# Kernel tuning notes

Hardware: AMD Instinct MI355X
Metric: run time of the kernel (lower is better)

The kernel has to match this reference:

```python
import jax, jax.numpy as jnp
import numpy as np

B, L, D = 8, 512, 256


def hard_sigmoid(x):
    # Keras 1.x default inner_activation for LSTM gates
    return jnp.clip(0.2 * x + 0.5, 0.0, 1.0)


def lstm_step(x_t, h, c, W, U, b):
    # gates in Keras order: i, f, g(candidate), o
    z = x_t @ W + h @ U + b  # (B, 4D)
    i, f, g, o = jnp.split(z, 4, axis=-1)
    i = hard_sigmoid(i)
    f = hard_sigmoid(f)
    g = jnp.tanh(g)
    o = hard_sigmoid(o)
    c_new = f * c + i * g
    h_new = o * jnp.tanh(c_new)
    return h_new, c_new


def setup_inputs() -> dict:
    key = jax.random.key(0)
    ks = jax.random.split(key, 10)
    s = 1.0 / np.sqrt(D)
    x = jax.random.normal(ks[0], (B, L, D), dtype=jnp.float32)
    W_r = jax.random.normal(ks[1], (D, 4 * D), dtype=jnp.float32) * s
    U_r = jax.random.normal(ks[2], (D, 4 * D), dtype=jnp.float32) * s
    b_r = jnp.zeros((4 * D,), dtype=jnp.float32)
    W_w = jax.random.normal(ks[3], (D, 4 * D), dtype=jnp.float32) * s
    U_w = jax.random.normal(ks[4], (D, 4 * D), dtype=jnp.float32) * s
    b_w = jnp.zeros((4 * D,), dtype=jnp.float32)
    W_c = jax.random.normal(ks[5], (2 * D, D), dtype=jnp.float32) * s
    b_c = jnp.zeros((D,), dtype=jnp.float32)
    return {"x": x, "W_r": W_r, "U_r": U_r, "b_r": b_r,
            "W_w": W_w, "U_w": U_w, "b_w": b_w, "W_c": W_c, "b_c": b_c}


def reference(x, W_r, U_r, b_r, W_w, U_w, b_w, W_c, b_c):
    Bb, Ll, Dd = x.shape
    h0 = jnp.zeros((Bb, Dd), dtype=x.dtype)

    # --- reader LSTM (return_sequences=True), eq. 1 ---
    def reader_step(carry, x_t):
        h, c = carry
        h, c = lstm_step(x_t, h, c, W_r, U_r, b_r)
        return (h, c), h

    _, o_seq = jax.lax.scan(reader_step, (h0, h0), jnp.swapaxes(x, 0, 1))  # (L, B, D)

    # --- compose-and-write loop, eqs. 2-6; mem_0 = x ---
    def write_step(carry, o_t):
        mem, h, c = carry  # mem: (B, L, D)
        z = jax.nn.softmax(jnp.einsum('bd,bld->bl', o_t, mem), axis=-1)  # (B, L)
        m_rt = jnp.einsum('bl,bld->bd', z, mem)                           # (B, D)
        c_t = jnp.concatenate([o_t, m_rt], axis=-1) @ W_c + b_c          # linear composer
        h_new, c_new = lstm_step(c_t, h, c, W_w, U_w, b_w)
        mem_new = mem * (1.0 - z[..., None]) + h_new[:, None, :] * z[..., None]
        return (mem_new, h_new, c_new), h_new

    (_, _, _), h_seq = jax.lax.scan(write_step, (x, h0, h0), o_seq)
    # return_mode == 'last_output'
    return h_seq[-1]
```

## Files before the change

kernel.cpp:

```cpp
#include <hip/hip_runtime.h>
#include <math.h>

#define BB 8
#define LL 512
#define DD 256
#define NG4 1024
#define WGB 32
#define WR 16
#define WU 8
#define MLD 264

typedef __attribute__((ext_vector_type(4))) float f32x4;

static const size_t OFF_XW    = 0;
static const size_t OFF_F     = OFF_XW + (size_t)BB*LL*NG4;
static const size_t OFF_BMW   = OFF_F + (size_t)DD*NG4;
static const size_t OFF_B2    = OFF_BMW + (size_t)DD*NG4;
static const size_t OFF_HR    = OFF_B2 + NG4;
static const size_t OFF_HW    = OFF_HR + (size_t)2*BB*DD;
static const size_t OFF_PMAX  = OFF_HW + (size_t)BB*DD;
static const size_t OFF_PSUM  = OFF_PMAX + (size_t)BB*WGB;
static const size_t OFF_PM    = OFF_PSUM + (size_t)BB*WGB;
static const size_t OFF_FLAGS = OFF_PM + (size_t)BB*WGB*DD;
static const size_t TOTAL_WS  = OFF_FLAGS + BB*WGB;

__device__ __forceinline__ float hsig(float x) {
    return fminf(fmaxf(0.2f*x + 0.5f, 0.0f), 1.0f);
}

__device__ __forceinline__ void st_coh(float* p, float v) {
    __hip_atomic_store(p, v, __ATOMIC_RELAXED, __HIP_MEMORY_SCOPE_AGENT);
}
__device__ __forceinline__ float ld_coh(const float* p) {
    return __hip_atomic_load(p, __ATOMIC_RELAXED, __HIP_MEMORY_SCOPE_AGENT);
}
__device__ __forceinline__ void st_coh_u(unsigned* p, unsigned v) {
    __hip_atomic_store(p, v, __ATOMIC_RELAXED, __HIP_MEMORY_SCOPE_AGENT);
}
__device__ __forceinline__ unsigned ld_coh_u(const unsigned* p) {
    return __hip_atomic_load(p, __ATOMIC_RELAXED, __HIP_MEMORY_SCOPE_AGENT);
}

__device__ __forceinline__ void ld_pm8(
    const f32x4* p0, const f32x4* p1, const f32x4* p2, const f32x4* p3,
    const f32x4* p4, const f32x4* p5, const f32x4* p6, const f32x4* p7,
    f32x4& a0, f32x4& a1, f32x4& a2, f32x4& a3,
    f32x4& a4, f32x4& a5, f32x4& a6, f32x4& a7)
{
    asm volatile(
        "global_load_dwordx4 %0, %8, off sc0 sc1\n\t"
        "global_load_dwordx4 %1, %9, off sc0 sc1\n\t"
        "global_load_dwordx4 %2, %10, off sc0 sc1\n\t"
        "global_load_dwordx4 %3, %11, off sc0 sc1\n\t"
        "global_load_dwordx4 %4, %12, off sc0 sc1\n\t"
        "global_load_dwordx4 %5, %13, off sc0 sc1\n\t"
        "global_load_dwordx4 %6, %14, off sc0 sc1\n\t"
        "global_load_dwordx4 %7, %15, off sc0 sc1\n\t"
        "s_waitcnt vmcnt(0)"
        : "=&v"(a0), "=&v"(a1), "=&v"(a2), "=&v"(a3),
          "=&v"(a4), "=&v"(a5), "=&v"(a6), "=&v"(a7)
        : "v"(p0), "v"(p1), "v"(p2), "v"(p3),
          "v"(p4), "v"(p5), "v"(p6), "v"(p7)
        : "memory");
}

__device__ __forceinline__ void flag_barrier(unsigned* flb, int wg, unsigned target, int tid) {
    asm volatile("s_waitcnt vmcnt(0)" ::: "memory");
    __syncthreads();
    if (tid == 0) st_coh_u(&flb[wg], target);
    if (tid < 64) {
        unsigned v;
        do {
            v = ld_coh_u(&flb[tid & 31]);
        } while (!__all(v >= target));
    }
    __syncthreads();
}

template<int TM, int TN, int TK>
__global__ void __launch_bounds__(256) gemm_nn(
    const float* __restrict__ A, int lda,
    const float* __restrict__ Bmat, int ldb,
    const float* __restrict__ bias,
    float* __restrict__ C, int ldc,
    int M, int N, int K)
{
    __shared__ float As[TK][TM];
    __shared__ float Bs[TK][TN];
    const int m0 = blockIdx.y * TM, n0 = blockIdx.x * TN;
    const int tid = threadIdx.x;
    const int tx = tid % (TN/4);
    const int ty = tid / (TN/4);
    float acc[4][4] = {};
    for (int k0 = 0; k0 < K; k0 += TK) {
        {
            const int e = tid*4;
            const int m = e / TK, k = e % TK;
            const float4 v = *reinterpret_cast<const float4*>(&A[(size_t)(m0+m)*lda + k0 + k]);
            As[k+0][m] = v.x; As[k+1][m] = v.y; As[k+2][m] = v.z; As[k+3][m] = v.w;
        }
        {
            const int e = tid*4;
            const int k = e / TN, n = e % TN;
            const float4 v = *reinterpret_cast<const float4*>(&Bmat[(size_t)(k0+k)*ldb + n0 + n]);
            Bs[k][n+0] = v.x; Bs[k][n+1] = v.y; Bs[k][n+2] = v.z; Bs[k][n+3] = v.w;
        }
        __syncthreads();
        #pragma unroll
        for (int kk = 0; kk < TK; ++kk) {
            float a[4], bv[4];
            #pragma unroll
            for (int i = 0; i < 4; ++i) a[i] = As[kk][ty*4+i];
            #pragma unroll
            for (int j = 0; j < 4; ++j) bv[j] = Bs[kk][tx*4+j];
            #pragma unroll
            for (int i = 0; i < 4; ++i)
                #pragma unroll
                for (int j = 0; j < 4; ++j) acc[i][j] += a[i]*bv[j];
        }
        __syncthreads();
    }
    #pragma unroll
    for (int i = 0; i < 4; ++i) {
        const int m = m0 + ty*4 + i;
        #pragma unroll
        for (int j = 0; j < 4; ++j) {
            const int n = n0 + tx*4 + j;
            C[(size_t)m*ldc + n] = acc[i][j] + (bias ? bias[n] : 0.0f);
        }
    }
}

__global__ void __launch_bounds__(256) b2_kernel(
    const float* __restrict__ bc, const float* __restrict__ Ww,
    const float* __restrict__ bw, float* __restrict__ B2)
{
    const int n = blockIdx.x*256 + threadIdx.x;
    float a = bw[n];
    for (int k = 0; k < DD; ++k) a += bc[k]*Ww[(size_t)k*NG4 + n];
    B2[n] = a;
}

__global__ void __launch_bounds__(256) fused_kernel(
    const float* __restrict__ XW, const float* __restrict__ Fw,
    const float* __restrict__ Bm, const float* __restrict__ B2,
    const float* __restrict__ Ur, const float* __restrict__ Uw,
    const float* __restrict__ x,
    float* __restrict__ HR, float* __restrict__ HWb,
    float* __restrict__ PMAX, float* __restrict__ PSUM, float* __restrict__ PM,
    unsigned* __restrict__ flags, float* __restrict__ out)
{
    extern __shared__ float sm[];
    float* Urs  = sm;
    float* Uws  = Urs + 8192;
    float* Fs   = Uws + 8192;
    float* Bms  = Fs + 8192;
    float* mems = Bms + 8192;
    float* hr   = mems + WR*MLD;
    float* hw   = hr + 256;
    float* ms   = hw + 256;
    float* zredR= ms + 256;
    float* zredW= zredR + 256;
    float* red4 = zredW + 256;
    float* xws  = red4 + 1024;
    float* zrs  = xws + 32;
    float* g1s  = zrs + 32;
    float* zws  = g1s + 32;
    float* b2s  = zws + 32;
    float* fwS  = b2s + 32;
    float* ssx  = fwS + 32;
    float* esx  = ssx + 16;
    float* cr   = esx + 16;
    float* cw   = cr + 8;
    float* misc = cw + 8;

    const int b   = (int)blockIdx.x & 7;
    const int wg  = (int)blockIdx.x >> 3;
    const int tid = threadIdx.x;
    const int R0  = wg*WR;
    const int U0  = wg*WU;

    for (int it = 0; it < 32; ++it) {
        const int e = it*256 + tid;
        const int k = e >> 5, cl = e & 31;
        const int gc = (cl>>3)*DD + U0 + (cl&7);
        Urs[k*32+cl] = Ur[(size_t)k*NG4 + gc];
        Uws[k*32+cl] = Uw[(size_t)k*NG4 + gc];
        Fs [k*32+cl] = Fw[(size_t)k*NG4 + gc];
        Bms[k*32+cl] = Bm[(size_t)k*NG4 + gc];
    }
    if (tid < 32) b2s[tid] = B2[(tid>>3)*DD + U0 + (tid&7)];
    for (int r = 0; r < WR; ++r)
        mems[r*MLD + tid] = x[((size_t)b*LL + R0 + r)*DD + tid];
    if (tid < 8) { cr[tid] = 0.f; cw[tid] = 0.f; }
    __syncthreads();

    unsigned* flb = flags + b*WGB;

    for (int s = 0; s <= LL; ++s) {
        const bool doR = (s < LL), doW = (s >= 1);

        if (doR && tid < 32)
            xws[tid] = XW[((size_t)b*LL + s)*NG4 + (tid>>3)*DD + U0 + (tid&7)];
        hr[tid] = (s >= 1) ? ld_coh(&HR[((size_t)((s-1)&1))*BB*DD + b*DD + tid]) : 0.f;
        hw[tid] = (s >= 2) ? ld_coh(&HWb[b*DD + tid]) : 0.f;
        __syncthreads();

        if (s >= 2) {
            const float scale = misc[0];
            const float hwd = hw[tid];
            #pragma unroll
            for (int r = 0; r < WR; ++r) {
                const float z = esx[r]*scale;
                float* mp = &mems[r*MLD + tid];
                *mp = *mp*(1.f - z) + hwd*z;
            }
        }
        __syncthreads();

        if (doW) {
            const int r = tid >> 4, j = tid & 15;
            float a = 0.f;
            const float* mrow = mems + r*MLD;
            #pragma unroll 4
            for (int d = j; d < DD; d += 16) a += hr[d]*mrow[d];
            #pragma unroll
            for (int off = 8; off; off >>= 1) a += __shfl_down(a, off, 16);
            if (j == 0) ssx[r] = a;
        }
        {
            const int kc = tid >> 5, cl = tid & 31;
            const int k0 = kc*32;
            float aR = 0.f, aW = 0.f;
            #pragma unroll 8
            for (int k = k0; k < k0+32; ++k) {
                aR += hr[k]*Urs[k*32+cl];
                aW += hw[k]*Uws[k*32+cl] + hr[k]*Fs[k*32+cl];
            }
            zredR[tid] = aR; zredW[tid] = aW;
        }
        __syncthreads();

        if (tid < 16) {
            const float v = ssx[tid];
            float m = v;
            #pragma unroll
            for (int off = 8; off; off >>= 1) m = fmaxf(m, __shfl_xor(m, off, 16));
            const float e = __expf(v - m);
            esx[tid] = e;
            float sum = e;
            #pragma unroll
            for (int off = 8; off; off >>= 1) sum += __shfl_xor(sum, off, 16);
            if (tid == 0 && doW) {
                st_coh(&PMAX[b*WGB + wg], m);
                st_coh(&PSUM[b*WGB + wg], sum);
            }
        } else if (tid >= 64 && tid < 96) {
            const int cl = tid - 64;
            float z = xws[cl];
            #pragma unroll
            for (int q = 0; q < 8; ++q) z += zredR[q*32 + cl];
            zrs[cl] = z;
        } else if (tid >= 128 && tid < 160) {
            const int cl = tid - 128;
            float z = b2s[cl];
            #pragma unroll
            for (int q = 0; q < 8; ++q) z += zredW[q*32 + cl];
            g1s[cl] = z;
        }
        __syncthreads();

        if (doW) {
            float p = 0.f;
            #pragma unroll
            for (int r = 0; r < WR; ++r) p += esx[r]*mems[r*MLD + tid];
            st_coh(&PM[((size_t)b*WGB + wg)*DD + tid], p);
        }
        if (doR && tid < 8) {
            const float ig = hsig(zrs[tid]);
            const float fg = hsig(zrs[8+tid]);
            const float gg = tanhf(zrs[16+tid]);
            const float og = hsig(zrs[24+tid]);
            const float c  = fg*cr[tid] + ig*gg;
            cr[tid] = c;
            st_coh(&HR[((size_t)(s&1))*BB*DD + b*DD + U0 + tid], og*tanhf(c));
        }
        flag_barrier(flb, wg, 2u*(unsigned)s + 1u, tid);

        if (doW) {
            if (tid < 32) {
                const float pmx = ld_coh(&PMAX[b*WGB + tid]);
                const float ps  = ld_coh(&PSUM[b*WGB + tid]);
                float g = pmx;
                #pragma unroll
                for (int off = 16; off; off >>= 1) g = fmaxf(g, __shfl_xor(g, off, 32));
                const float fw = __expf(pmx - g);
                float S = ps*fw;
                #pragma unroll
                for (int off = 16; off; off >>= 1) S += __shfl_xor(S, off, 32);
                fwS[tid] = fw;
                if (tid == 0)  misc[1] = 1.f/S;
                if (tid == wg) misc[0] = fw/S;
            }
            __syncthreads();
            {
                const int w0 = tid >> 6, dq = tid & 63;
                const float* pmb = PM + (size_t)b*WGB*DD;
                const f32x4* p0 = (const f32x4*)(pmb + (w0+ 0)*DD) + dq;
                const f32x4* p1 = (const f32x4*)(pmb + (w0+ 4)*DD) + dq;
                const f32x4* p2 = (const f32x4*)(pmb + (w0+ 8)*DD) + dq;
                const f32x4* p3 = (const f32x4*)(pmb + (w0+12)*DD) + dq;
                const f32x4* p4 = (const f32x4*)(pmb + (w0+16)*DD) + dq;
                const f32x4* p5 = (const f32x4*)(pmb + (w0+20)*DD) + dq;
                const f32x4* p6 = (const f32x4*)(pmb + (w0+24)*DD) + dq;
                const f32x4* p7 = (const f32x4*)(pmb + (w0+28)*DD) + dq;
                f32x4 a0,a1,a2,a3,a4,a5,a6,a7;
                ld_pm8(p0,p1,p2,p3,p4,p5,p6,p7, a0,a1,a2,a3,a4,a5,a6,a7);
                f32x4 acc = a0*fwS[w0];
                acc += a1*fwS[w0+4];  acc += a2*fwS[w0+8];
                acc += a3*fwS[w0+12]; acc += a4*fwS[w0+16];
                acc += a5*fwS[w0+20]; acc += a6*fwS[w0+24];
                acc += a7*fwS[w0+28];
                *(f32x4*)(red4 + w0*DD + dq*4) = acc;
            }
            __syncthreads();
            ms[tid] = (red4[tid] + red4[DD+tid] + red4[2*DD+tid] + red4[3*DD+tid]) * misc[1];
            __syncthreads();
            {
                const int kc = tid >> 5, cl = tid & 31, k0 = kc*32;
                float a = 0.f;
                #pragma unroll 8
                for (int k = k0; k < k0+32; ++k) a += ms[k]*Bms[k*32+cl];
                zredW[tid] = a;
            }
            __syncthreads();
            if (tid < 32) {
                float z = g1s[tid];
                #pragma unroll
                for (int q = 0; q < 8; ++q) z += zredW[q*32 + tid];
                zws[tid] = z;
            }
            __syncthreads();
            if (tid < 8) {
                const float ig = hsig(zws[tid]);
                const float fg = hsig(zws[8+tid]);
                const float gg = tanhf(zws[16+tid]);
                const float og = hsig(zws[24+tid]);
                const float c  = fg*cw[tid] + ig*gg;
                cw[tid] = c;
                const float h = og*tanhf(c);
                st_coh(&HWb[b*DD + U0 + tid], h);
                if (s == LL) out[b*DD + U0 + tid] = h;
            }
        }
        if (s < LL) flag_barrier(flb, wg, 2u*(unsigned)s + 2u, tid);
    }
}

extern "C" void kernel_launch(void* const* d_in, const int* in_sizes, int n_in,
                              void* d_out, int out_size, void* d_ws, size_t ws_size,
                              hipStream_t stream) {
    const float* x   = (const float*)d_in[0];
    const float* W_r = (const float*)d_in[1];
    const float* U_r = (const float*)d_in[2];
    const float* b_r = (const float*)d_in[3];
    const float* W_w = (const float*)d_in[4];
    const float* U_w = (const float*)d_in[5];
    const float* b_w = (const float*)d_in[6];
    const float* W_c = (const float*)d_in[7];
    const float* b_c = (const float*)d_in[8];
    (void)in_sizes; (void)n_in;

    if (ws_size < TOTAL_WS * sizeof(float)) return;

    float* ws   = (float*)d_ws;
    float* XW   = ws + OFF_XW;
    float* Fmat = ws + OFF_F;
    float* Bmw  = ws + OFF_BMW;
    float* B2   = ws + OFF_B2;
    float* HR   = ws + OFF_HR;
    float* HWb  = ws + OFF_HW;
    float* PMAX = ws + OFF_PMAX;
    float* PSUM = ws + OFF_PSUM;
    float* PM   = ws + OFF_PM;
    unsigned* flags = (unsigned*)(ws + OFF_FLAGS);

    const int FUSED_LDS = 39540 * 4;
    hipFuncSetAttribute((const void*)fused_kernel, hipFuncAttributeMaxDynamicSharedMemorySize, FUSED_LDS);

    hipMemsetAsync(flags, 0, BB*WGB*sizeof(unsigned), stream);

    dim3 blk(256);
    gemm_nn<64,64,16><<<dim3(NG4/64, (BB*LL)/64), blk, 0, stream>>>(
        x, DD, W_r, NG4, b_r, XW, NG4, BB*LL, NG4, DD);
    gemm_nn<64,64,16><<<dim3(NG4/64, DD/64), blk, 0, stream>>>(
        W_c, DD, W_w, NG4, nullptr, Fmat, NG4, DD, NG4, DD);
    gemm_nn<64,64,16><<<dim3(NG4/64, DD/64), blk, 0, stream>>>(
        W_c + (size_t)DD*DD, DD, W_w, NG4, nullptr, Bmw, NG4, DD, NG4, DD);
    b2_kernel<<<dim3(NG4/256), blk, 0, stream>>>(b_c, W_w, b_w, B2);
    fused_kernel<<<dim3(BB*WGB), blk, FUSED_LDS, stream>>>(
        XW, Fmat, Bmw, B2, U_r, U_w, x, HR, HWb, PMAX, PSUM, PM, flags, (float*)d_out);
}
```

Baseline: 4.711 ms.

## Restructure fused LSTM step to overlap reader with writer and shorten barrier paths

Reorganizes the per-step schedule of the persistent fused kernel. The reader LSTM runs one step ahead, and its first step is computed directly at setup. The attention score is computed algebraically from the previous dot product plus a single h·hw reduction, which avoids reading the updated memory first. The memory update is moved into the flag-barrier wait window, and the global loads for PM, PMAX/PSUM, HR and XW are issued right after the barrier so they overlap. The aim is to take LDS passes and barrier latency off the serial critical path, at the cost of more complex indexing and a higher risk of subtle ordering or correctness bugs.

```diff
diff --git a/kernel.cpp b/kernel.cpp
--- a/kernel.cpp
+++ b/kernel.cpp
@@ -64,19 +64,6 @@
         : "memory");
 }
 
-__device__ __forceinline__ void flag_barrier(unsigned* flb, int wg, unsigned target, int tid) {
-    asm volatile("s_waitcnt vmcnt(0)" ::: "memory");
-    __syncthreads();
-    if (tid == 0) st_coh_u(&flb[wg], target);
-    if (tid < 64) {
-        unsigned v;
-        do {
-            v = ld_coh_u(&flb[tid & 31]);
-        } while (!__all(v >= target));
-    }
-    __syncthreads();
-}
-
 template<int TM, int TN, int TK>
 __global__ void __launch_bounds__(256) gemm_nn(
     const float* __restrict__ A, int lda,
@@ -156,21 +143,23 @@
     float* Fs   = Uws + 8192;
     float* Bms  = Fs + 8192;
     float* mems = Bms + 8192;
-    float* hr   = mems + WR*MLD;
-    float* hw   = hr + 256;
+    float* hr2  = mems + WR*MLD;
+    float* hw   = hr2 + 512;
     float* ms   = hw + 256;
     float* zredR= ms + 256;
     float* zredW= zredR + 256;
     float* red4 = zredW + 256;
     float* xws  = red4 + 1024;
-    float* zrs  = xws + 32;
-    float* g1s  = zrs + 32;
-    float* zws  = g1s + 32;
-    float* b2s  = zws + 32;
-    float* fwS  = b2s + 32;
-    float* ssx  = fwS + 32;
-    float* esx  = ssx + 16;
-    float* cr   = esx + 16;
+    float* b2s  = xws + 32;
+    float* zrs  = b2s + 32;
+    float* zws  = zrs + 32;
+    float* fwS  = zws + 32;
+    float* d1   = fwS + 32;
+    float* zp   = d1 + 16;
+    float* esx  = zp + 16;
+    float* wv   = esx + 16;
+    float* wsum = wv + 16;
+    float* cr   = wsum + 8;
     float* cw   = cr + 8;
     float* misc = cw + 8;
 
@@ -179,6 +168,7 @@
     const int tid = threadIdx.x;
     const int R0  = wg*WR;
     const int U0  = wg*WU;
+    const int gc32 = (tid>>3)*DD + U0 + (tid&7);
 
     for (int it = 0; it < 32; ++it) {
         const int e = it*256 + tid;
@@ -189,113 +179,123 @@
         Fs [k*32+cl] = Fw[(size_t)k*NG4 + gc];
         Bms[k*32+cl] = Bm[(size_t)k*NG4 + gc];
     }
-    if (tid < 32) b2s[tid] = B2[(tid>>3)*DD + U0 + (tid&7)];
+    if (tid < 32) b2s[tid] = B2[gc32];
     for (int r = 0; r < WR; ++r)
         mems[r*MLD + tid] = x[((size_t)b*LL + R0 + r)*DD + tid];
-    if (tid < 8) { cr[tid] = 0.f; cw[tid] = 0.f; }
+    {
+        const size_t base = (size_t)b*LL*NG4;
+        const float zi = XW[base + tid];
+        const float zg = XW[base + 512 + tid];
+        const float zo = XW[base + 768 + tid];
+        const float c0 = hsig(zi)*tanhf(zg);
+        hr2[tid] = hsig(zo)*tanhf(c0);
+        hr2[256 + tid] = 0.f;
+        if (tid >= U0 && tid < U0+WU) cr[tid-U0] = c0;
+    }
+    if (tid < 16) { zp[tid] = 0.f; d1[tid] = 0.f; esx[tid] = 0.f; }
+    if (tid < 8)  cw[tid] = 0.f;
+    if (tid < 4)  misc[tid] = 0.f;
     __syncthreads();
 
     unsigned* flb = flags + b*WGB;
 
     for (int s = 0; s <= LL; ++s) {
-        const bool doR = (s < LL), doW = (s >= 1);
-
-        if (doR && tid < 32)
-            xws[tid] = XW[((size_t)b*LL + s)*NG4 + (tid>>3)*DD + U0 + (tid&7)];
-        hr[tid] = (s >= 1) ? ld_coh(&HR[((size_t)((s-1)&1))*BB*DD + b*DD + tid]) : 0.f;
-        hw[tid] = (s >= 2) ? ld_coh(&HWb[b*DD + tid]) : 0.f;
-        __syncthreads();
-
-        if (s >= 2) {
-            const float scale = misc[0];
-            const float hwd = hw[tid];
-            #pragma unroll
-            for (int r = 0; r < WR; ++r) {
-                const float z = esx[r]*scale;
-                float* mp = &mems[r*MLD + tid];
-                *mp = *mp*(1.f - z) + hwd*z;
-            }
-        }
-        __syncthreads();
-
-        if (doW) {
-            const int r = tid >> 4, j = tid & 15;
-            float a = 0.f;
-            const float* mrow = mems + r*MLD;
-            #pragma unroll 4
-            for (int d = j; d < DD; d += 16) a += hr[d]*mrow[d];
-            #pragma unroll
-            for (int off = 8; off; off >>= 1) a += __shfl_down(a, off, 16);
-            if (j == 0) ssx[r] = a;
-        }
+        const bool doW = (s >= 1);
+        float* hrN_s = hr2 + (s&1)*256;
+        float* hrO_s = hr2 + ((s+1)&1)*256;
+
+        float hw_r = 0.f;
+        if (s >= 2) hw_r = ld_coh(&HWb[b*DD + tid]);
+        hw[tid] = hw_r;
+        __syncthreads();
+
         {
-            const int kc = tid >> 5, cl = tid & 31;
-            const int k0 = kc*32;
-            float aR = 0.f, aW = 0.f;
-            #pragma unroll 8
-            for (int k = k0; k < k0+32; ++k) {
-                aR += hr[k]*Urs[k*32+cl];
-                aW += hw[k]*Uws[k*32+cl] + hr[k]*Fs[k*32+cl];
-            }
-            zredR[tid] = aR; zredW[tid] = aW;
-        }
-        __syncthreads();
-
-        if (tid < 16) {
-            const float v = ssx[tid];
-            float m = v;
+            float v = hrO_s[tid]*hw_r;
+            #pragma unroll
+            for (int off = 32; off; off >>= 1) v += __shfl_xor(v, off);
+            if ((tid & 63) == 0) wsum[tid>>6] = v;
+        }
+        __syncthreads();
+
+        if (doW && tid < 16) {
+            const float d2v = wsum[0]+wsum[1]+wsum[2]+wsum[3];
+            const float zpv = zp[tid];
+            const float sc  = (1.f - zpv)*d1[tid] + zpv*d2v;
+            float m = sc;
             #pragma unroll
             for (int off = 8; off; off >>= 1) m = fmaxf(m, __shfl_xor(m, off, 16));
-            const float e = __expf(v - m);
+            const float e = __expf(sc - m);
             esx[tid] = e;
-            float sum = e;
-            #pragma unroll
-            for (int off = 8; off; off >>= 1) sum += __shfl_xor(sum, off, 16);
-            if (tid == 0 && doW) {
+            wv[tid]  = e*(1.f - zpv);
+            float sum = e, bp = e*zpv;
+            #pragma unroll
+            for (int off = 8; off; off >>= 1) {
+                sum += __shfl_xor(sum, off, 16);
+                bp  += __shfl_xor(bp,  off, 16);
+            }
+            if (tid == 0) {
+                misc[2] = bp;
                 st_coh(&PMAX[b*WGB + wg], m);
                 st_coh(&PSUM[b*WGB + wg], sum);
             }
-        } else if (tid >= 64 && tid < 96) {
-            const int cl = tid - 64;
-            float z = xws[cl];
-            #pragma unroll
-            for (int q = 0; q < 8; ++q) z += zredR[q*32 + cl];
-            zrs[cl] = z;
-        } else if (tid >= 128 && tid < 160) {
-            const int cl = tid - 128;
-            float z = b2s[cl];
-            #pragma unroll
-            for (int q = 0; q < 8; ++q) z += zredW[q*32 + cl];
-            g1s[cl] = z;
         }
         __syncthreads();
 
         if (doW) {
-            float p = 0.f;
-            #pragma unroll
-            for (int r = 0; r < WR; ++r) p += esx[r]*mems[r*MLD + tid];
+            float p = misc[2]*hw_r;
+            #pragma unroll
+            for (int r = 0; r < WR; ++r) p += wv[r]*mems[r*MLD + tid];
             st_coh(&PM[((size_t)b*WGB + wg)*DD + tid], p);
         }
-        if (doR && tid < 8) {
-            const float ig = hsig(zrs[tid]);
-            const float fg = hsig(zrs[8+tid]);
-            const float gg = tanhf(zrs[16+tid]);
-            const float og = hsig(zrs[24+tid]);
-            const float c  = fg*cr[tid] + ig*gg;
-            cr[tid] = c;
-            st_coh(&HR[((size_t)(s&1))*BB*DD + b*DD + U0 + tid], og*tanhf(c));
-        }
-        flag_barrier(flb, wg, 2u*(unsigned)s + 1u, tid);
+
+        asm volatile("s_waitcnt vmcnt(0)" ::: "memory");
+        __syncthreads();
+        if (tid == 0) st_coh_u(&flb[wg], 2u*(unsigned)s + 1u);
+        if (s >= 2) {
+            #pragma unroll
+            for (int r = 0; r < WR; ++r) {
+                const float z = zp[r];
+                float* mp = &mems[r*MLD + tid];
+                *mp = *mp*(1.f - z) + hw_r*z;
+            }
+        }
+        if (tid < 64) {
+            const unsigned target = 2u*(unsigned)s + 1u;
+            unsigned v;
+            do { v = ld_coh_u(&flb[tid & 31]); } while (!__all(v >= target));
+        }
+        __syncthreads();
+
+        float hrN_r = 0.f;
+        if (s >= 1 && s <= 511) hrN_r = ld_coh(&HR[((size_t)(s&1))*BB*DD + b*DD + tid]);
+        float xw_r = 0.f;
+        if (s <= 510 && tid < 32) xw_r = XW[((size_t)b*LL + s + 1)*NG4 + gc32];
+        float pmx_r = 0.f, ps_r = 0.f;
+        if (doW && tid < 32) {
+            pmx_r = ld_coh(&PMAX[b*WGB + tid]);
+            ps_r  = ld_coh(&PSUM[b*WGB + tid]);
+        }
+        f32x4 a0,a1,a2,a3,a4,a5,a6,a7;
+        const int w0 = tid >> 6, dq = tid & 63;
+        if (doW) {
+            const float* pmb = PM + (size_t)b*WGB*DD;
+            ld_pm8((const f32x4*)(pmb + (w0+ 0)*DD) + dq, (const f32x4*)(pmb + (w0+ 4)*DD) + dq,
+                   (const f32x4*)(pmb + (w0+ 8)*DD) + dq, (const f32x4*)(pmb + (w0+12)*DD) + dq,
+                   (const f32x4*)(pmb + (w0+16)*DD) + dq, (const f32x4*)(pmb + (w0+20)*DD) + dq,
+                   (const f32x4*)(pmb + (w0+24)*DD) + dq, (const f32x4*)(pmb + (w0+28)*DD) + dq,
+                   a0,a1,a2,a3,a4,a5,a6,a7);
+        }
+        if (s >= 1 && s <= 511) hrN_s[tid] = hrN_r;
+        if (s <= 510 && tid < 32) xws[tid] = xw_r;
+        __syncthreads();
 
         if (doW) {
             if (tid < 32) {
-                const float pmx = ld_coh(&PMAX[b*WGB + tid]);
-                const float ps  = ld_coh(&PSUM[b*WGB + tid]);
-                float g = pmx;
+                float g = pmx_r;
                 #pragma unroll
                 for (int off = 16; off; off >>= 1) g = fmaxf(g, __shfl_xor(g, off, 32));
-                const float fw = __expf(pmx - g);
-                float S = ps*fw;
+                const float fw = __expf(pmx_r - g);
+                float S = ps_r*fw;
                 #pragma unroll
                 for (int off = 16; off; off >>= 1) S += __shfl_xor(S, off, 32);
                 fwS[tid] = fw;
@@ -304,18 +304,6 @@
             }
             __syncthreads();
             {
-                const int w0 = tid >> 6, dq = tid & 63;
-                const float* pmb = PM + (size_t)b*WGB*DD;
-                const f32x4* p0 = (const f32x4*)(pmb + (w0+ 0)*DD) + dq;
-                const f32x4* p1 = (const f32x4*)(pmb + (w0+ 4)*DD) + dq;
-                const f32x4* p2 = (const f32x4*)(pmb + (w0+ 8)*DD) + dq;
-                const f32x4* p3 = (const f32x4*)(pmb + (w0+12)*DD) + dq;
-                const f32x4* p4 = (const f32x4*)(pmb + (w0+16)*DD) + dq;
-                const f32x4* p5 = (const f32x4*)(pmb + (w0+20)*DD) + dq;
-                const f32x4* p6 = (const f32x4*)(pmb + (w0+24)*DD) + dq;
-                const f32x4* p7 = (const f32x4*)(pmb + (w0+28)*DD) + dq;
-                f32x4 a0,a1,a2,a3,a4,a5,a6,a7;
-                ld_pm8(p0,p1,p2,p3,p4,p5,p6,p7, a0,a1,a2,a3,a4,a5,a6,a7);
                 f32x4 acc = a0*fwS[w0];
                 acc += a1*fwS[w0+4];  acc += a2*fwS[w0+8];
                 acc += a3*fwS[w0+12]; acc += a4*fwS[w0+16];
@@ -325,17 +313,19 @@
             }
             __syncthreads();
             ms[tid] = (red4[tid] + red4[DD+tid] + red4[2*DD+tid] + red4[3*DD+tid]) * misc[1];
+            if (tid < 16) zp[tid] = esx[tid]*misc[0];
             __syncthreads();
             {
                 const int kc = tid >> 5, cl = tid & 31, k0 = kc*32;
                 float a = 0.f;
                 #pragma unroll 8
-                for (int k = k0; k < k0+32; ++k) a += ms[k]*Bms[k*32+cl];
+                for (int k = k0; k < k0+32; ++k)
+                    a += hw[k]*Uws[k*32+cl] + hrO_s[k]*Fs[k*32+cl] + ms[k]*Bms[k*32+cl];
                 zredW[tid] = a;
             }
             __syncthreads();
             if (tid < 32) {
-                float z = g1s[tid];
+                float z = b2s[tid];
                 #pragma unroll
                 for (int q = 0; q < 8; ++q) z += zredW[q*32 + tid];
                 zws[tid] = z;
@@ -353,7 +343,53 @@
                 if (s == LL) out[b*DD + U0 + tid] = h;
             }
         }
-        if (s < LL) flag_barrier(flb, wg, 2u*(unsigned)s + 2u, tid);
+
+        if (s <= 510) {
+            const int kc = tid >> 5, cl = tid & 31, k0 = kc*32;
+            float a = 0.f;
+            #pragma unroll 8
+            for (int k = k0; k < k0+32; ++k) a += hrN_s[k]*Urs[k*32+cl];
+            zredR[tid] = a;
+        }
+        __syncthreads();
+        if (s <= 510 && tid < 32) {
+            float z = xws[tid];
+            #pragma unroll
+            for (int q = 0; q < 8; ++q) z += zredR[q*32 + tid];
+            zrs[tid] = z;
+        }
+        __syncthreads();
+        if (s <= 510 && tid < 8) {
+            const float ig = hsig(zrs[tid]);
+            const float fg = hsig(zrs[8+tid]);
+            const float gg = tanhf(zrs[16+tid]);
+            const float og = hsig(zrs[24+tid]);
+            const float c  = fg*cr[tid] + ig*gg;
+            cr[tid] = c;
+            st_coh(&HR[((size_t)((s+1)&1))*BB*DD + b*DD + U0 + tid], og*tanhf(c));
+        }
+        if (s < LL) {
+            const int r = tid >> 4, j = tid & 15;
+            float a = 0.f;
+            const float* mrow = mems + r*MLD;
+            #pragma unroll 4
+            for (int d = j; d < DD; d += 16) a += hrN_s[d]*mrow[d];
+            #pragma unroll
+            for (int off = 8; off; off >>= 1) a += __shfl_down(a, off, 16);
+            if (j == 0) d1[r] = a;
+        }
+
+        if (s < LL) {
+            asm volatile("s_waitcnt vmcnt(0)" ::: "memory");
+            __syncthreads();
+            if (tid == 0) st_coh_u(&flb[wg], 2u*(unsigned)s + 2u);
+            if (tid < 64) {
+                const unsigned target = 2u*(unsigned)s + 2u;
+                unsigned v;
+                do { v = ld_coh_u(&flb[tid & 31]); } while (!__all(v >= target));
+            }
+            __syncthreads();
+        }
     }
 }
 
@@ -385,7 +421,7 @@
     float* PM   = ws + OFF_PM;
     unsigned* flags = (unsigned*)(ws + OFF_FLAGS);
 
-    const int FUSED_LDS = 39540 * 4;
+    const int FUSED_LDS = 39808 * 4;
     hipFuncSetAttribute((const void*)fused_kernel, hipFuncAttributeMaxDynamicSharedMemorySize, FUSED_LDS);
 
     hipMemsetAsync(flags, 0, BB*WGB*sizeof(unsigned), stream);
```

Result: faster. 4.373 ms (-7.2%).
